# Kernel tuning notes

Hardware: AMD Instinct MI355X
Metric: run time of the kernel (lower is better)

## Reference

```python
import jax, jax.numpy as jnp
import numpy as np

DIST_THRESHOLD = 2.0
CONF_SIGMA = 1.0


def setup_inputs() -> dict:
    key = jax.random.key(0)
    k1, k2 = jax.random.split(key)
    pred_points = jax.random.normal(k1, (1024, 20, 2), dtype=jnp.float32)
    gt_points = jax.random.normal(k2, (2048, 20, 2), dtype=jnp.float32)
    return {"pred_points": pred_points, "gt_points": gt_points}


def reference(pred_points, gt_points):
    # pred_points: (N, P, 2), gt_points: (M, P, 2)
    # simple distance: mean over P of per-point Euclidean distance -> (N, M)
    diff = pred_points[:, None, :, :] - gt_points[None, :, :, :]  # (N, M, P, 2)
    distances = jnp.sqrt(jnp.sum(diff * diff, axis=-1)).mean(axis=-1)  # (N, M)
    min_distances = distances.min(axis=1)          # (N,)
    matched_indices = distances.argmin(axis=1)     # (N,) int
    matched_points = gt_points[matched_indices]    # (N, P, 2)
    confidence = jnp.where(
        min_distances > DIST_THRESHOLD,
        jnp.float32(0.0),
        jnp.exp(-min_distances / CONF_SIGMA),
    )[:, None]                                     # (N, 1)
    return matched_points, confidence, matched_indices
```

## Files before the change

### kernel.cpp

```cpp
#include <hip/hip_runtime.h>

#define N 1024
#define M 2048
#define P 20
#define THREADS 256
#define WAVES 4
#define CHUNKS 128
#define GROUPS 16
#define RPC (M / CHUNKS)
#define RPW (RPC / WAVES)
#define PSTRIDE 41

typedef unsigned long long u64;


__global__ __launch_bounds__(THREADS) void pm_partial(
    const float* __restrict__ pred, const float* __restrict__ gt,
    u64* __restrict__ best)
{
    const int tid   = threadIdx.x;
    const int wave  = tid >> 6;
    const int lane  = tid & 63;
    const int chunk = blockIdx.x;
    const int group = blockIdx.y;

    __shared__ float s_pred[64 * PSTRIDE];
    {
        const float4* psrc = (const float4*)(pred + group * 64 * 40);
        for (int t = tid; t < 64 * 10; t += THREADS) {
            float4 v = psrc[t];
            const int r = t / 10, j = t - r * 10;
            float* dst = &s_pred[r * PSTRIDE + 4 * j];
            dst[0] = v.x; dst[1] = v.y; dst[2] = v.z; dst[3] = v.w;
        }
    }
    __syncthreads();

    float pr[40];
#pragma unroll
    for (int e = 0; e < 40; ++e) pr[e] = s_pred[lane * PSTRIDE + e];

    float bd = 3.4e38f;
    int   bi = 0x7fffffff;
    const int m0 = chunk * RPC + wave * RPW;
#pragma unroll 2
    for (int r = 0; r < RPW; ++r) {
        const int m_u = __builtin_amdgcn_readfirstlane(m0 + r);
        const float4* gp = (const float4*)(gt + m_u * 40);
        float acc = 0.0f;
#pragma unroll
        for (int q = 0; q < 10; ++q) {
            float4 g = gp[q];
            float dx0 = pr[4*q+0] - g.x;
            float dy0 = pr[4*q+1] - g.y;
            float dx1 = pr[4*q+2] - g.z;
            float dy1 = pr[4*q+3] - g.w;
            acc += __builtin_amdgcn_sqrtf(dx0*dx0 + dy0*dy0);
            acc += __builtin_amdgcn_sqrtf(dx1*dx1 + dy1*dy1);
        }
        float dist = acc * (1.0f / P);
        if (dist < bd) { bd = dist; bi = m_u; }
    }

    u64 key = ((u64)__float_as_uint(bd) << 32) | (unsigned)bi;

    __shared__ u64 s_k[WAVES][64];
    s_k[wave][lane] = key;
    __syncthreads();
    if (wave == 0) {
        u64 k = s_k[0][lane];
#pragma unroll
        for (int w = 1; w < WAVES; ++w) {
            u64 o = s_k[w][lane];
            if (o < k) k = o;
        }
        atomicMin(&best[group * 64 + lane], k);
    }
}

__global__ __launch_bounds__(256) void pm_final(
    const float* __restrict__ gt, const u64* __restrict__ best,
    float* __restrict__ out)
{
    const int tid = threadIdx.x;
    const int blk = blockIdx.x;
    __shared__ int s_fi[64];

    if (tid < 64) {
        const int n = blk * 64 + tid;
        u64 k = best[n];
        float fd = __uint_as_float((unsigned)(k >> 32));
        int   fi = (int)(unsigned)(k & 0xffffffffu);
        out[40960 + n] = (fd > 2.0f) ? 0.0f : expf(-fd);
        out[41984 + n] = (float)fi;
        s_fi[tid] = fi;
    }
    __syncthreads();

    const int base_row = blk * 64;
    for (int t = tid; t < 64 * 40; t += 256) {
        const int r = t / 40;
        const int e = t - r * 40;
        out[(base_row + r) * 40 + e] = gt[s_fi[r] * 40 + e];
    }
}

extern "C" void kernel_launch(void* const* d_in, const int* in_sizes, int n_in,
                              void* d_out, int out_size, void* d_ws, size_t ws_size,
                              hipStream_t stream) {
    const float* pred = (const float*)d_in[0];
    const float* gt   = (const float*)d_in[1];
    float* out = (float*)d_out;
    u64*  best = (u64*)d_ws;
    (void)in_sizes; (void)n_in; (void)out_size; (void)ws_size;

    dim3 grid1(CHUNKS, GROUPS);
    pm_partial<<<grid1, THREADS, 0, stream>>>(pred, gt, best);
    pm_final<<<N / 64, 256, 0, stream>>>(gt, best, out);
}
```

Measured before the change: 70.21 us.

## Fuse partial and final kernels via last-block-done atomic counter

Merges the two launches into one kernel. Each block bumps a global counter after its atomicMin, and the block that finishes last runs the whole finalization: confidence, index output and the gathered copy of matched gt rows for all 1024 predictions. This removes the second launch and the gap between the two kernels. In exchange the final gather is serialized onto a single 256-thread block, and correctness depends on the workspace counter being pre-filled with a specific poison value on every call.

```diff
diff --git a/kernel.cpp b/kernel.cpp
--- a/kernel.cpp
+++ b/kernel.cpp
@@ -10,13 +10,17 @@
 #define RPC (M / CHUNKS)
 #define RPW (RPC / WAVES)
 #define PSTRIDE 41
+#define NBLOCKS (CHUNKS * GROUPS)
 
 typedef unsigned long long u64;
 
 
-__global__ __launch_bounds__(THREADS) void pm_partial(
+#define CTR_POISON 0xAAAAAAAAu
+
+__global__ __launch_bounds__(THREADS) void pm_fused(
     const float* __restrict__ pred, const float* __restrict__ gt,
-    u64* __restrict__ best)
+    u64* __restrict__ best, unsigned* __restrict__ done,
+    float* __restrict__ out)
 {
     const int tid   = threadIdx.x;
     const int wave  = tid >> 6;
@@ -76,32 +80,32 @@
         }
         atomicMin(&best[group * 64 + lane], k);
     }
-}
 
-__global__ __launch_bounds__(256) void pm_final(
-    const float* __restrict__ gt, const u64* __restrict__ best,
-    float* __restrict__ out)
-{
-    const int tid = threadIdx.x;
-    const int blk = blockIdx.x;
-    __shared__ int s_fi[64];
+    __shared__ int s_last;
+    __threadfence();
+    if (tid == 0) {
+        unsigned old = atomicAdd(done, 1u);
+        s_last = (old == CTR_POISON + (unsigned)(NBLOCKS - 1)) ? 1 : 0;
+    }
+    __syncthreads();
+    if (!s_last) return;
+    __threadfence();
 
-    if (tid < 64) {
-        const int n = blk * 64 + tid;
-        u64 k = best[n];
+    __shared__ int s_fi[N];
+    for (int n = tid; n < N; n += THREADS) {
+        u64 k = atomicMin(&best[n], ~0ull);
         float fd = __uint_as_float((unsigned)(k >> 32));
         int   fi = (int)(unsigned)(k & 0xffffffffu);
         out[40960 + n] = (fd > 2.0f) ? 0.0f : expf(-fd);
         out[41984 + n] = (float)fi;
-        s_fi[tid] = fi;
+        s_fi[n] = fi;
     }
     __syncthreads();
 
-    const int base_row = blk * 64;
-    for (int t = tid; t < 64 * 40; t += 256) {
+    for (int t = tid; t < N * 40; t += THREADS) {
         const int r = t / 40;
         const int e = t - r * 40;
-        out[(base_row + r) * 40 + e] = gt[s_fi[r] * 40 + e];
+        out[r * 40 + e] = gt[s_fi[r] * 40 + e];
     }
 }
 
@@ -112,9 +116,9 @@
     const float* gt   = (const float*)d_in[1];
     float* out = (float*)d_out;
     u64*  best = (u64*)d_ws;
+    unsigned* done = (unsigned*)((char*)d_ws + 8192);
     (void)in_sizes; (void)n_in; (void)out_size; (void)ws_size;
 
-    dim3 grid1(CHUNKS, GROUPS);
-    pm_partial<<<grid1, THREADS, 0, stream>>>(pred, gt, best);
-    pm_final<<<N / 64, 256, 0, stream>>>(gt, best, out);
+    dim3 grid(CHUNKS, GROUPS);
+    pm_fused<<<grid, THREADS, 0, stream>>>(pred, gt, best, done, out);
 }
```

Measured after the change: 189.8 us. 2.7x slower.
